# Performance work log

Measured on AMD Instinct MI355X. Metric: run time of the kernel, lower is better.

Reference implementation:

```python
import jax, jax.numpy as jnp
import numpy as np

K_NEIGHBORS = 16
NUM_PATCHES = 32
W_NORMAL = 1.0
W_SURFVAR = 1.0


def _knn_centered(points, k):
    """points: [B, N, 3] -> k nearest neighbors re-centered at each point, [B, N, k, 3].
    Distances are computed on stop_gradient(points) to match torch's .detach()."""
    pd = jax.lax.stop_gradient(points)
    # squared pairwise distances [B, N, N] (sqrt is monotone -> topk order identical)
    d2 = jnp.sum((pd[:, :, None, :] - pd[:, None, :, :]) ** 2, axis=-1)
    _, idx = jax.lax.top_k(-d2, k)  # smallest-k indices, [B, N, k]
    knn = jax.vmap(lambda pts, id_: pts[id_])(points, idx)  # [B, N, k, 3]
    return knn - points[:, :, None, :]


def _eig_props(knn):
    """knn: [B, N, k, 3] -> (normal [B,N,3] = eigvec of smallest eigval, eigvals [B,N,3] ascending)."""
    cov = jnp.einsum('bnki,bnkj->bnij', knn, knn)  # [B, N, 3, 3]
    w, v = jnp.linalg.eigh(cov)  # ascending eigenvalues, matches torch.symeig
    return v[..., :, 0], w


def setup_inputs() -> dict:
    key = jax.random.key(0)
    pointCloud = jax.random.normal(key, (4, 8192, 3), dtype=jnp.float32)
    return {"pointCloud": pointCloud}


def reference(pointCloud):
    B, N, _ = pointCloud.shape
    pp = N // NUM_PATCHES

    # global kNN / normals / surface variance
    knn_g = _knn_centered(pointCloud, K_NEIGHBORS)
    nrm_g, w_g = _eig_props(knn_g)

    # patchwise: each patch is an independent small point cloud -> fold patches into batch
    patch_pts = pointCloud.reshape(B * NUM_PATCHES, pp, 3)
    knn_p = _knn_centered(patch_pts, K_NEIGHBORS)
    nrm_p, w_p = _eig_props(knn_p)
    nrm_p = nrm_p.reshape(B, N, 3)

    # normal loss (abs variant, sign-ambiguity-free)
    loss_n = jnp.mean(jnp.linalg.norm(jnp.abs(nrm_p) - jnp.abs(nrm_g), axis=2)) * W_NORMAL

    # surface variance loss: lambda_min / sum(lambda)
    sv_g = w_g[..., 0] / jnp.sum(w_g, axis=-1)            # [B, N]
    sv_p = (w_p[..., 0] / jnp.sum(w_p, axis=-1)).reshape(B, N)
    loss_sv = jnp.mean((sv_p - sv_g) ** 2) * W_SURFVAR

    return jnp.stack([loss_n, loss_sv])  # [2] (original returns list of two [1] tensors)
```

## Files before the change

kernel.cpp:

```cpp
#include <hip/hip_runtime.h>
#include <math.h>

#define KNN 16
#define NPTS 8192
#define PTCH 256
#define NPATCH 32
#define NBATCH 4
#define SSTRIDE 130
#define LAMBDA_T 48.0f

#define NC 16
#define NCELLS (NC * NC * NC)
#define GMIN -4.2f
#define ICS 1.9047619f

__device__ __forceinline__ float lam_f(float r, float s)
{
    const float C     = 0.063493636f;
    const float SQ2PI = 2.5066283f;
    const float IS2   = 0.70710678f;
    float a = fabsf(r - s), b = r + s;
    float amr = a - r;
    float coefA = amr * amr + 2.f - s * s;
    float I = 2.f * __expf(-0.5f * b * b) - coefA * __expf(-0.5f * a * a)
            + r * SQ2PI * (erff(b * IS2) - erff(a * IS2));
    float M = C * (3.14159265f / r) * I;
    if (s > r) {
        float u = s - r;
        M += 12.566371f * C * (1.2533141f * erff(u * IS2) - u * __expf(-0.5f * u * u));
    }
    return (float)NPTS * M;
}

__device__ __forceinline__ void jrot(double& app, double& aqq, double& apq,
                                     double& arp, double& arq,
                                     double& vp0, double& vq0,
                                     double& vp1, double& vq1,
                                     double& vp2, double& vq2)
{
    double g = apq;
    if (g == 0.0) return;
    double theta = (aqq - app) / (2.0 * g);
    double at = fabs(theta);
    double t = (at > 1.0e154) ? (0.5 / theta)
                              : (copysign(1.0, theta) / (at + sqrt(theta * theta + 1.0)));
    double c = 1.0 / sqrt(t * t + 1.0);
    double s = t * c;
    double tau = s / (1.0 + c);
    app -= t * g;
    aqq += t * g;
    apq = 0.0;
    double rp = arp, rq = arq;
    arp = rp - s * (rq + tau * rp);
    arq = rq + s * (rp - tau * rq);
    double p0 = vp0, q0 = vq0;
    vp0 = p0 - s * (q0 + tau * p0); vq0 = q0 + s * (p0 - tau * q0);
    double p1 = vp1, q1 = vq1;
    vp1 = p1 - s * (q1 + tau * p1); vq1 = q1 + s * (p1 - tau * q1);
    double p2 = vp2, q2 = vq2;
    vp2 = p2 - s * (q2 + tau * p2); vq2 = q2 + s * (p2 - tau * q2);
}

__device__ __forceinline__ void eig3(double a00, double a11, double a22,
                                     double a01, double a02, double a12,
                                     double& nx, double& ny, double& nz,
                                     double& lmin, double& lsum)
{
    double v00 = 1, v01 = 0, v02 = 0;
    double v10 = 0, v11 = 1, v12 = 0;
    double v20 = 0, v21 = 0, v22 = 1;
    double scale = fabs(a00) + fabs(a11) + fabs(a22) + fabs(a01) + fabs(a02) + fabs(a12);
    if (scale > 0.0) {
        for (int sweep = 0; sweep < 6; ++sweep) {
            double off = fabs(a01) + fabs(a02) + fabs(a12);
            if (off <= scale * 1e-15) break;
            jrot(a00, a11, a01, a02, a12, v00, v01, v10, v11, v20, v21);
            jrot(a00, a22, a02, a01, a12, v00, v02, v10, v12, v20, v22);
            jrot(a11, a22, a12, a01, a02, v01, v02, v11, v12, v21, v22);
        }
    }
    lsum = a00 + a11 + a22;
    lmin = a00; nx = v00; ny = v10; nz = v20;
    if (a11 < lmin) { lmin = a11; nx = v01; ny = v11; nz = v21; }
    if (a22 < lmin) { lmin = a22; nx = v02; ny = v12; nz = v22; }
}

__device__ __forceinline__ unsigned mkkey(float d2, unsigned idx) {
    return (__float_as_uint(d2) & 0xFFFFE000u) | idx;
}

__device__ __forceinline__ void insert16(unsigned key, unsigned* L)
{
    L[KNN - 1] = key;
    #pragma unroll
    for (int m = KNN - 1; m >= 1; --m) {
        unsigned a = L[m - 1], b = L[m];
        L[m - 1] = min(a, b);
        L[m]     = max(a, b);
    }
}

__device__ __forceinline__ void merge4(unsigned* L, int lane)
{
    #pragma unroll
    for (int step = 1; step <= 2; step <<= 1) {
        unsigned tmp[KNN];
        #pragma unroll
        for (int m = 0; m < KNN; ++m) tmp[m] = __shfl(L[m], lane ^ step, 64);
        for (int m = 0; m < KNN; ++m) {
            if (tmp[m] >= L[KNN - 1]) break;
            insert16(tmp[m], L);
        }
    }
}

__device__ __forceinline__ unsigned mbcnt64(unsigned long long m) {
    return __builtin_amdgcn_mbcnt_hi((unsigned)(m >> 32),
           __builtin_amdgcn_mbcnt_lo((unsigned)m, 0u));
}

__device__ __forceinline__ int cidx(float v) {
    int i = (int)floorf((v - GMIN) * ICS);
    return min(max(i, 0), NC - 1);
}
__device__ __forceinline__ int cellOf(float x, float y, float z) {
    return (cidx(z) * NC + cidx(y)) * NC + cidx(x);
}

#define BT 1024
__global__ void __launch_bounds__(1024)
build_kernel(const float* __restrict__ pts, float* __restrict__ out,
             unsigned* __restrict__ cellStart, float4* __restrict__ sorted)
{
    __shared__ unsigned hist[NCELLS];
    __shared__ unsigned part[BT];
    const int b = blockIdx.x;
    const int t = threadIdx.x;
    if (b == 0 && t == 0) { out[0] = 0.0f; out[1] = 0.0f; }
    for (int i = t; i < NCELLS; i += BT) hist[i] = 0u;
    __syncthreads();
    const float* base = pts + (size_t)b * (NPTS * 3);
    float px[8], py[8], pz[8];
    int pc[8];
    #pragma unroll
    for (int k = 0; k < 8; ++k) {
        int i = k * BT + t;
        px[k] = base[i * 3 + 0];
        py[k] = base[i * 3 + 1];
        pz[k] = base[i * 3 + 2];
        pc[k] = cellOf(px[k], py[k], pz[k]);
        atomicAdd(&hist[pc[k]], 1u);
    }
    __syncthreads();
    unsigned loc[4], s = 0;
    #pragma unroll
    for (int i = 0; i < 4; ++i) { loc[i] = s; s += hist[t * 4 + i]; }
    part[t] = s;
    __syncthreads();
    for (int o = 1; o < BT; o <<= 1) {
        unsigned u = (t >= o) ? part[t - o] : 0u;
        __syncthreads();
        part[t] += u;
        __syncthreads();
    }
    unsigned basex = part[t] - s;
    unsigned* csb = cellStart + b * (NCELLS + 1);
    #pragma unroll
    for (int i = 0; i < 4; ++i) {
        unsigned e = basex + loc[i];
        csb[t * 4 + i] = e;
        hist[t * 4 + i] = e;
    }
    if (t == BT - 1) csb[NCELLS] = basex + s;
    __syncthreads();
    float4* sb = sorted + (size_t)b * NPTS;
    #pragma unroll
    for (int k = 0; k < 8; ++k) {
        int i = k * BT + t;
        unsigned slot = atomicAdd(&hist[pc[k]], 1u);
        float4 v;
        v.x = px[k]; v.y = py[k]; v.z = pz[k]; v.w = __uint_as_float((unsigned)i);
        sb[slot] = v;
    }
}

__global__ void __launch_bounds__(256)
gate_kernel(const float* __restrict__ pts, float* __restrict__ g2buf)
{
    int q = blockIdx.x * 256 + threadIdx.x;
    int b = q >> 13, i = q & (NPTS - 1);
    const float* pp = pts + (size_t)b * (NPTS * 3) + (size_t)i * 3;
    float x = pp[0], y = pp[1], z = pp[2];
    float r = fmaxf(sqrtf(x * x + y * y + z * z), 0.01f);
    float lo = 0.f, hi = 12.f;
    #pragma unroll 1
    for (int it = 0; it < 16; ++it) {
        float mid = 0.5f * (lo + hi);
        if (lam_f(r, mid) < LAMBDA_T) lo = mid; else hi = mid;
    }
    g2buf[q] = hi * hi;
}

__global__ void __launch_bounds__(256)
fselect_kernel(const float* __restrict__ pts, const float* __restrict__ g2buf,
               const unsigned* __restrict__ cellStart,
               const float4* __restrict__ sortedp,
               unsigned* __restrict__ idx16)
{
    __shared__ unsigned survl[4 * SSTRIDE];
    const int t = threadIdx.x;
    const int wv = t >> 6;
    const int lane = t & 63;
    const int wq = __builtin_amdgcn_readfirstlane(blockIdx.x * 4 + wv);
    const int b  = wq >> 13;
    const int qi = wq & (NPTS - 1);
    const float* base = pts + (size_t)b * (NPTS * 3);
    const unsigned* cs = cellStart + b * (NCELLS + 1);
    const float4* sp = sortedp + (size_t)b * NPTS;
    unsigned* sl = survl + wv * SSTRIDE;

    const float qx = base[qi * 3 + 0];
    const float qy = base[qi * 3 + 1];
    const float qz = base[qi * 3 + 2];
    const float g2 = g2buf[wq];
    const float g  = sqrtf(g2);

    int ixlo = cidx(qx - g), ixhi = cidx(qx + g);
    int iylo = cidx(qy - g), iyhi = cidx(qy + g);
    int izlo = cidx(qz - g), izhi = cidx(qz + g);
    int nx = ixhi - ixlo + 1;
    int ny = iyhi - iylo + 1;
    int nyz = ny * (izhi - izlo + 1);
    const int lR  = (nyz >= 8) ? 3 : (nyz >= 4) ? 2 : (nyz >= 2) ? 1 : 0;
    const int R   = 1 << lR;
    const int lsl = 6 - lR;
    const unsigned SL = 64u >> lR;
    const unsigned slot = (unsigned)lane & (SL - 1u);
    unsigned cnt = 0;
    #pragma unroll 1
    for (int r0 = 0; r0 < nyz; r0 += 64) {
        int r = r0 + lane;
        unsigned pk = 0;
        if (r < nyz) {
            int iz = izlo + r / ny;
            int iy = iylo + (r - (r / ny) * ny);
            int cb = (iz * NC + iy) * NC + ixlo;
            unsigned sB = cs[cb];
            pk = sB | ((cs[cb + nx] - sB) << 14);
        }
        int rmax = min(nyz - r0, 64);
        int gcount = (rmax + R - 1) >> lR;
        #pragma unroll 1
        for (int gg = 0; gg < gcount; ++gg) {
            unsigned pkm = __shfl(pk, (gg << lR) + (lane >> lsl), 64);
            unsigned sBm = pkm & 0x3FFFu;
            unsigned lm  = pkm >> 14;
            #pragma unroll 1
            for (unsigned st = slot; ; st += SL) {
                bool in = st < lm;
                if (!__any(in ? 1 : 0)) break;
                float4 c = sp[min(sBm + st, (unsigned)(NPTS - 1))];
                float dx = qx - c.x, dy = qy - c.y, dz = qz - c.z;
                float d2 = dx * dx + dy * dy + dz * dz;
                bool pass = in && (d2 < g2);
                unsigned long long m = __ballot(pass);
                if (pass) {
                    unsigned sw = min(cnt + mbcnt64(m), (unsigned)(SSTRIDE - 1));
                    sl[sw] = mkkey(d2, __float_as_uint(c.w));
                }
                cnt += (unsigned)__popcll(m);
            }
        }
    }

    bool valid = (cnt >= KNN) && (cnt <= 128u);
    if (valid) {
        unsigned k0 = (lane < (int)cnt)      ? sl[lane]      : 0xFFFFFFFFu;
        unsigned k1 = (lane + 64 < (int)cnt) ? sl[lane + 64] : 0xFFFFFFFFu;
        unsigned P = 0;
        #pragma unroll 1
        for (int bit = 31; bit >= 0; --bit) {
            unsigned mid = P | (1u << bit);
            unsigned c = (unsigned)__popcll(__ballot(k0 < mid))
                       + (unsigned)__popcll(__ballot(k1 < mid));
            if (c < 16u) P = mid;
        }
        float upper = __uint_as_float((P & 0xFFFFE000u) + 0x2000u);
        valid = (upper < g2 * 0.999f - 1e-5f);
        if (valid) {
            bool sel0 = (k0 <= P);
            bool sel1 = (k1 <= P);
            unsigned long long m0 = __ballot(sel0);
            unsigned long long m1 = __ballot(sel1);
            unsigned base1 = (unsigned)__popcll(m0);
            if (sel0) sl[mbcnt64(m0)] = k0;
            if (sel1) sl[base1 + mbcnt64(m1)] = k1;
            unsigned myk = sl[lane & 15];
            unsigned rnk = 0;
            #pragma unroll
            for (int j = 0; j < 16; ++j) {
                unsigned kj = __shfl(myk, j, 64);
                rnk += (kj < myk) ? 1u : 0u;
            }
            if (lane < 16)
                idx16[(size_t)wq * 32 + rnk] = myk & 0x1FFFu;
        }
    }
    if (!valid && lane == 0) {
        unsigned gl[KNN];
        #pragma unroll
        for (int m = 0; m < KNN; ++m) gl[m] = 0xFFFFFFFFu;
        #pragma unroll 1
        for (int i = 0; i < NPTS; ++i) {
            float cx = base[i * 3 + 0];
            float cy = base[i * 3 + 1];
            float cz = base[i * 3 + 2];
            float dx = qx - cx, dy = qy - cy, dz = qz - cz;
            float d2 = dx * dx + dy * dy + dz * dz;
            unsigned k = mkkey(d2, (unsigned)i);
            if (k < gl[KNN - 1]) insert16(k, gl);
        }
        unsigned* dst = idx16 + (size_t)wq * 32;
        #pragma unroll
        for (int m = 0; m < KNN; ++m) dst[m] = gl[m] & 0x1FFFu;
    }
}

__global__ void __launch_bounds__(256)
pselect_kernel(const float* __restrict__ pts, unsigned* __restrict__ idx16)
{
    __shared__ float4 pbuf4[PTCH];
    const int t = threadIdx.x;
    const int w = t >> 6;
    const int lane = t & 63;
    const int p = blockIdx.x;
    const int quarter = blockIdx.y;
    const int b = blockIdx.z;
    const float* base = pts + (size_t)b * (NPTS * 3);

    {
        const float* src = base + p * (PTCH * 3);
        float* dst = (float*)pbuf4;
        #pragma unroll
        for (int s = 0; s < 3; ++s) {
            int f = t + s * 256;
            int j = f / 3;
            int c = f - 3 * j;
            dst[j * 4 + c] = src[f];
        }
    }
    __syncthreads();

    const int qq = lane >> 2;
    const int h = lane & 3;
    const int qlocal = quarter * 64 + w * 16 + qq;
    float4 qv = pbuf4[qlocal];
    const float pqx = qv.x, pqy = qv.y, pqz = qv.z;

    unsigned pl[KNN];
    #pragma unroll
    for (int m = 0; m < KNN; ++m) pl[m] = 0xFFFFFFFFu;
    const int j0 = h * 64;
    #pragma unroll 4
    for (int j = j0; j < j0 + 64; ++j) {
        float4 c = pbuf4[j];
        float dx = pqx - c.x, dy = pqy - c.y, dz = pqz - c.z;
        float d2 = dx * dx + dy * dy + dz * dz;
        unsigned k = mkkey(d2, (unsigned)j);
        if (k < pl[KNN - 1]) insert16(k, pl);
    }
    merge4(pl, lane);
    if (h == 0) {
        int qid = b * NPTS + p * PTCH + qlocal;
        unsigned* dst = idx16 + (size_t)qid * 32 + 16;
        #pragma unroll
        for (int m = 0; m < KNN; ++m)
            dst[m] = (unsigned)(p * PTCH) + (pl[m] & 0x1FFFu);
    }
}

__global__ void __launch_bounds__(256)
eig_loss_kernel(const float* __restrict__ pts,
                const unsigned* __restrict__ idx16,
                double* __restrict__ partials)
{
    __shared__ double sln[4], slv[4];
    const int t = threadIdx.x;
    const int e = blockIdx.x * 256 + t;
    const int qid = e >> 1;
    const int b = qid >> 13;
    const int qi = qid & (NPTS - 1);
    const float* base = pts + (size_t)b * (NPTS * 3);

    const double qxd = (double)base[qi * 3 + 0];
    const double qyd = (double)base[qi * 3 + 1];
    const double qzd = (double)base[qi * 3 + 2];

    const unsigned* L = idx16 + (size_t)qid * 32 + (e & 1) * 16;
    double c00 = 0, c11 = 0, c22 = 0, c01 = 0, c02 = 0, c12 = 0;
    #pragma unroll
    for (int m = 0; m < KNN; ++m) {
        int idx = (int)L[m];
        double dx = (double)base[idx * 3 + 0] - qxd;
        double dy = (double)base[idx * 3 + 1] - qyd;
        double dz = (double)base[idx * 3 + 2] - qzd;
        c00 += dx * dx; c11 += dy * dy; c22 += dz * dz;
        c01 += dx * dy; c02 += dx * dz; c12 += dy * dz;
    }
    double nx, ny, nz, lmin, lsum;
    eig3(c00, c11, c22, c01, c02, c12, nx, ny, nz, lmin, lsum);
    double sv = lmin / lsum;

    double onx = __shfl_xor(nx, 1, 64);
    double ony = __shfl_xor(ny, 1, 64);
    double onz = __shfl_xor(nz, 1, 64);
    double osv = __shfl_xor(sv, 1, 64);

    double ln = 0.0, lsv = 0.0;
    if ((e & 1) == 0) {
        double dx = fabs(onx) - fabs(nx);
        double dy = fabs(ony) - fabs(ny);
        double dz = fabs(onz) - fabs(nz);
        ln  = sqrt(dx * dx + dy * dy + dz * dz);
        double ds = osv - sv;
        lsv = ds * ds;
    }
    #pragma unroll
    for (int o = 32; o > 0; o >>= 1) {
        ln  += __shfl_down(ln, o);
        lsv += __shfl_down(lsv, o);
    }
    const int w = t >> 6;
    if ((t & 63) == 0) { sln[w] = ln; slv[w] = lsv; }
    __syncthreads();
    if (t == 0) {
        partials[blockIdx.x * 2 + 0] = sln[0] + sln[1] + sln[2] + sln[3];
        partials[blockIdx.x * 2 + 1] = slv[0] + slv[1] + slv[2] + slv[3];
    }
}

__global__ void __launch_bounds__(256)
reduce_kernel(const double* __restrict__ partials, float* __restrict__ out)
{
    __shared__ double sln[4], slv[4];
    const int t = threadIdx.x;
    double a = partials[t * 2 + 0];
    double c = partials[t * 2 + 1];
    #pragma unroll
    for (int o = 32; o > 0; o >>= 1) {
        a += __shfl_down(a, o);
        c += __shfl_down(c, o);
    }
    if ((t & 63) == 0) { sln[t >> 6] = a; slv[t >> 6] = c; }
    __syncthreads();
    if (t == 0) {
        const double inv = 1.0 / (double)(NBATCH * NPTS);
        out[0] = (float)((sln[0] + sln[1] + sln[2] + sln[3]) * inv);
        out[1] = (float)((slv[0] + slv[1] + slv[2] + slv[3]) * inv);
    }
}

extern "C" void kernel_launch(void* const* d_in, const int* in_sizes, int n_in,
                              void* d_out, int out_size, void* d_ws, size_t ws_size,
                              hipStream_t stream)
{
    const float* pts = (const float*)d_in[0];
    float* out = (float*)d_out;

    unsigned char* ws = (unsigned char*)d_ws;
    unsigned* cellStart = (unsigned*)(ws);
    float4*   sorted    = (float4*)  (ws + 65552);
    float*    g2buf     = (float*)   (ws + 589840);
    unsigned* idx16     = (unsigned*)(ws + 720912);
    double*   partials  = (double*)  (ws + 4915216);

    hipLaunchKernelGGL(build_kernel, dim3(NBATCH), dim3(BT), 0, stream,
                       pts, out, cellStart, sorted);
    hipLaunchKernelGGL(gate_kernel, dim3(NBATCH * NPTS / 256), dim3(256), 0, stream,
                       pts, g2buf);
    hipLaunchKernelGGL(fselect_kernel, dim3(NBATCH * NPTS / 4), dim3(256), 0, stream,
                       pts, g2buf, cellStart, sorted, idx16);
    hipLaunchKernelGGL(pselect_kernel, dim3(NPATCH, 4, NBATCH), dim3(256), 0, stream,
                       pts, idx16);
    hipLaunchKernelGGL(eig_loss_kernel, dim3(NBATCH * NPTS * 2 / 256), dim3(256),
                       0, stream, pts, idx16, partials);
    hipLaunchKernelGGL(reduce_kernel, dim3(1), dim3(256), 0, stream,
                       partials, out);
}
```

Measured before the change: 146.4 us.

## Split grid build into parallel count/scan/scatter and process queries in cell order

```diff
diff --git a/kernel.cpp b/kernel.cpp
--- a/kernel.cpp
+++ b/kernel.cpp
@@ -127,61 +127,58 @@
     return (cidx(z) * NC + cidx(y)) * NC + cidx(x);
 }
 
-#define BT 1024
-__global__ void __launch_bounds__(1024)
-build_kernel(const float* __restrict__ pts, float* __restrict__ out,
-             unsigned* __restrict__ cellStart, float4* __restrict__ sorted)
-{
-    __shared__ unsigned hist[NCELLS];
-    __shared__ unsigned part[BT];
-    const int b = blockIdx.x;
-    const int t = threadIdx.x;
-    if (b == 0 && t == 0) { out[0] = 0.0f; out[1] = 0.0f; }
-    for (int i = t; i < NCELLS; i += BT) hist[i] = 0u;
-    __syncthreads();
-    const float* base = pts + (size_t)b * (NPTS * 3);
-    float px[8], py[8], pz[8];
-    int pc[8];
-    #pragma unroll
-    for (int k = 0; k < 8; ++k) {
-        int i = k * BT + t;
-        px[k] = base[i * 3 + 0];
-        py[k] = base[i * 3 + 1];
-        pz[k] = base[i * 3 + 2];
-        pc[k] = cellOf(px[k], py[k], pz[k]);
-        atomicAdd(&hist[pc[k]], 1u);
-    }
-    __syncthreads();
-    unsigned loc[4], s = 0;
-    #pragma unroll
-    for (int i = 0; i < 4; ++i) { loc[i] = s; s += hist[t * 4 + i]; }
+__global__ void __launch_bounds__(256) count_kernel(const float* __restrict__ pts,
+                                                    unsigned* __restrict__ counts)
+{
+    int gid = blockIdx.x * 256 + threadIdx.x;
+    int b = gid >> 13, i = gid & (NPTS - 1);
+    const float* p = pts + (size_t)b * (NPTS * 3) + (size_t)i * 3;
+    atomicAdd(&counts[b * NCELLS + cellOf(p[0], p[1], p[2])], 1u);
+}
+
+__global__ void __launch_bounds__(256) scan_kernel(const unsigned* __restrict__ counts,
+                                                   unsigned* __restrict__ cellStart,
+                                                   unsigned* __restrict__ cellPos)
+{
+    __shared__ unsigned part[256];
+    const int b = blockIdx.x, t = threadIdx.x;
+    const unsigned* cnt = counts + b * NCELLS;
+    unsigned loc[16], s = 0;
+    #pragma unroll
+    for (int i = 0; i < 16; ++i) { loc[i] = s; s += cnt[t * 16 + i]; }
     part[t] = s;
     __syncthreads();
-    for (int o = 1; o < BT; o <<= 1) {
+    for (int o = 1; o < 256; o <<= 1) {
         unsigned u = (t >= o) ? part[t - o] : 0u;
         __syncthreads();
         part[t] += u;
         __syncthreads();
     }
-    unsigned basex = part[t] - s;
+    unsigned base = part[t] - s;
     unsigned* csb = cellStart + b * (NCELLS + 1);
-    #pragma unroll
-    for (int i = 0; i < 4; ++i) {
-        unsigned e = basex + loc[i];
-        csb[t * 4 + i] = e;
-        hist[t * 4 + i] = e;
-    }
-    if (t == BT - 1) csb[NCELLS] = basex + s;
-    __syncthreads();
-    float4* sb = sorted + (size_t)b * NPTS;
-    #pragma unroll
-    for (int k = 0; k < 8; ++k) {
-        int i = k * BT + t;
-        unsigned slot = atomicAdd(&hist[pc[k]], 1u);
-        float4 v;
-        v.x = px[k]; v.y = py[k]; v.z = pz[k]; v.w = __uint_as_float((unsigned)i);
-        sb[slot] = v;
-    }
+    unsigned* cpb = cellPos + b * NCELLS;
+    #pragma unroll
+    for (int i = 0; i < 16; ++i) {
+        unsigned e = base + loc[i];
+        csb[t * 16 + i] = e;
+        cpb[t * 16 + i] = e;
+    }
+    if (t == 255) csb[NCELLS] = base + s;
+}
+
+__global__ void __launch_bounds__(256) scatter_kernel(const float* __restrict__ pts,
+                                                      unsigned* __restrict__ cellPos,
+                                                      float4* __restrict__ sorted)
+{
+    int gid = blockIdx.x * 256 + threadIdx.x;
+    int b = gid >> 13, i = gid & (NPTS - 1);
+    const float* p = pts + (size_t)b * (NPTS * 3) + (size_t)i * 3;
+    float x = p[0], y = p[1], z = p[2];
+    int c = cellOf(x, y, z);
+    unsigned slot = atomicAdd(&cellPos[b * NCELLS + c], 1u);
+    float4 v;
+    v.x = x; v.y = y; v.z = z; v.w = __uint_as_float((unsigned)i);
+    sorted[(size_t)b * NPTS + slot] = v;
 }
 
 __global__ void __launch_bounds__(256)
@@ -212,17 +209,17 @@
     const int wv = t >> 6;
     const int lane = t & 63;
     const int wq = __builtin_amdgcn_readfirstlane(blockIdx.x * 4 + wv);
-    const int b  = wq >> 13;
-    const int qi = wq & (NPTS - 1);
+    const int b   = wq >> 13;
+    const int pos = wq & (NPTS - 1);
     const float* base = pts + (size_t)b * (NPTS * 3);
     const unsigned* cs = cellStart + b * (NCELLS + 1);
     const float4* sp = sortedp + (size_t)b * NPTS;
     unsigned* sl = survl + wv * SSTRIDE;
 
-    const float qx = base[qi * 3 + 0];
-    const float qy = base[qi * 3 + 1];
-    const float qz = base[qi * 3 + 2];
-    const float g2 = g2buf[wq];
+    const float4 qc = sp[pos];
+    const float qx = qc.x, qy = qc.y, qz = qc.z;
+    const int oq = b * NPTS + (int)__float_as_uint(qc.w);
+    const float g2 = g2buf[oq];
     const float g  = sqrtf(g2);
 
     int ixlo = cidx(qx - g), ixhi = cidx(qx + g);
@@ -303,7 +300,7 @@
                 rnk += (kj < myk) ? 1u : 0u;
             }
             if (lane < 16)
-                idx16[(size_t)wq * 32 + rnk] = myk & 0x1FFFu;
+                idx16[(size_t)oq * 32 + rnk] = myk & 0x1FFFu;
         }
     }
     if (!valid && lane == 0) {
@@ -320,7 +317,7 @@
             unsigned k = mkkey(d2, (unsigned)i);
             if (k < gl[KNN - 1]) insert16(k, gl);
         }
-        unsigned* dst = idx16 + (size_t)wq * 32;
+        unsigned* dst = idx16 + (size_t)oq * 32;
         #pragma unroll
         for (int m = 0; m < KNN; ++m) dst[m] = gl[m] & 0x1FFFu;
     }
@@ -469,13 +466,20 @@
 
     unsigned char* ws = (unsigned char*)d_ws;
     unsigned* cellStart = (unsigned*)(ws);
-    float4*   sorted    = (float4*)  (ws + 65552);
-    float*    g2buf     = (float*)   (ws + 589840);
-    unsigned* idx16     = (unsigned*)(ws + 720912);
-    double*   partials  = (double*)  (ws + 4915216);
-
-    hipLaunchKernelGGL(build_kernel, dim3(NBATCH), dim3(BT), 0, stream,
-                       pts, out, cellStart, sorted);
+    unsigned* counts    = (unsigned*)(ws + 65552);
+    unsigned* cellPos   = (unsigned*)(ws + 131088);
+    float4*   sorted    = (float4*)  (ws + 196624);
+    float*    g2buf     = (float*)   (ws + 720912);
+    unsigned* idx16     = (unsigned*)(ws + 851984);
+    double*   partials  = (double*)  (ws + 5046288);
+
+    hipMemsetAsync(counts, 0, (size_t)NBATCH * NCELLS * sizeof(unsigned), stream);
+    hipLaunchKernelGGL(count_kernel, dim3(NBATCH * NPTS / 256), dim3(256), 0, stream,
+                       pts, counts);
+    hipLaunchKernelGGL(scan_kernel, dim3(NBATCH), dim3(256), 0, stream,
+                       counts, cellStart, cellPos);
+    hipLaunchKernelGGL(scatter_kernel, dim3(NBATCH * NPTS / 256), dim3(256), 0, stream,
+                       pts, cellPos, sorted);
     hipLaunchKernelGGL(gate_kernel, dim3(NBATCH * NPTS / 256), dim3(256), 0, stream,
                        pts, g2buf);
     hipLaunchKernelGGL(fselect_kernel, dim3(NBATCH * NPTS / 4), dim3(256), 0, stream,
```

After: 151.0 us. +3.2%, slower.

## Fuse gate radius search into fselect, process queries in cell order, rank-select top-16

Applied to the files above, without the earlier changes.

```diff
diff --git a/kernel.cpp b/kernel.cpp
--- a/kernel.cpp
+++ b/kernel.cpp
@@ -129,14 +129,13 @@
 
 #define BT 1024
 __global__ void __launch_bounds__(1024)
-build_kernel(const float* __restrict__ pts, float* __restrict__ out,
+build_kernel(const float* __restrict__ pts,
              unsigned* __restrict__ cellStart, float4* __restrict__ sorted)
 {
     __shared__ unsigned hist[NCELLS];
     __shared__ unsigned part[BT];
     const int b = blockIdx.x;
     const int t = threadIdx.x;
-    if (b == 0 && t == 0) { out[0] = 0.0f; out[1] = 0.0f; }
     for (int i = t; i < NCELLS; i += BT) hist[i] = 0u;
     __syncthreads();
     const float* base = pts + (size_t)b * (NPTS * 3);
@@ -185,24 +184,7 @@
 }
 
 __global__ void __launch_bounds__(256)
-gate_kernel(const float* __restrict__ pts, float* __restrict__ g2buf)
-{
-    int q = blockIdx.x * 256 + threadIdx.x;
-    int b = q >> 13, i = q & (NPTS - 1);
-    const float* pp = pts + (size_t)b * (NPTS * 3) + (size_t)i * 3;
-    float x = pp[0], y = pp[1], z = pp[2];
-    float r = fmaxf(sqrtf(x * x + y * y + z * z), 0.01f);
-    float lo = 0.f, hi = 12.f;
-    #pragma unroll 1
-    for (int it = 0; it < 16; ++it) {
-        float mid = 0.5f * (lo + hi);
-        if (lam_f(r, mid) < LAMBDA_T) lo = mid; else hi = mid;
-    }
-    g2buf[q] = hi * hi;
-}
-
-__global__ void __launch_bounds__(256)
-fselect_kernel(const float* __restrict__ pts, const float* __restrict__ g2buf,
+fselect_kernel(const float* __restrict__ pts,
                const unsigned* __restrict__ cellStart,
                const float4* __restrict__ sortedp,
                unsigned* __restrict__ idx16)
@@ -212,18 +194,27 @@
     const int wv = t >> 6;
     const int lane = t & 63;
     const int wq = __builtin_amdgcn_readfirstlane(blockIdx.x * 4 + wv);
-    const int b  = wq >> 13;
-    const int qi = wq & (NPTS - 1);
+    const int b   = wq >> 13;
+    const int pos = wq & (NPTS - 1);
     const float* base = pts + (size_t)b * (NPTS * 3);
     const unsigned* cs = cellStart + b * (NCELLS + 1);
     const float4* sp = sortedp + (size_t)b * NPTS;
     unsigned* sl = survl + wv * SSTRIDE;
 
-    const float qx = base[qi * 3 + 0];
-    const float qy = base[qi * 3 + 1];
-    const float qz = base[qi * 3 + 2];
-    const float g2 = g2buf[wq];
-    const float g  = sqrtf(g2);
+    const float4 qc = sp[pos];
+    const float qx = qc.x, qy = qc.y, qz = qc.z;
+    const int oq = b * NPTS + (int)__float_as_uint(qc.w);
+
+    const float r = fmaxf(sqrtf(qx * qx + qy * qy + qz * qz), 0.01f);
+    const float H1 = 12.0f / 64.0f;
+    float s1 = H1 * (float)(lane + 1);
+    unsigned j1 = (unsigned)__popcll(__ballot(lam_f(r, s1) < LAMBDA_T));
+    float lo1 = H1 * (float)min(j1, 63u);
+    const float H2 = H1 / 64.0f;
+    float s2 = lo1 + H2 * (float)(lane + 1);
+    unsigned j2 = (unsigned)__popcll(__ballot(lam_f(r, s2) < LAMBDA_T));
+    float g = lo1 + H2 * (float)(min(j2, 63u) + 1u);
+    const float g2 = g * g;
 
     int ixlo = cidx(qx - g), ixhi = cidx(qx + g);
     int iylo = cidx(qy - g), iyhi = cidx(qy + g);
@@ -239,11 +230,11 @@
     unsigned cnt = 0;
     #pragma unroll 1
     for (int r0 = 0; r0 < nyz; r0 += 64) {
-        int r = r0 + lane;
+        int rr = r0 + lane;
         unsigned pk = 0;
-        if (r < nyz) {
-            int iz = izlo + r / ny;
-            int iy = iylo + (r - (r / ny) * ny);
+        if (rr < nyz) {
+            int iz = izlo + rr / ny;
+            int iy = iylo + (rr - (rr / ny) * ny);
             int cb = (iz * NC + iy) * NC + ixlo;
             unsigned sB = cs[cb];
             pk = sB | ((cs[cb + nx] - sB) << 14);
@@ -277,33 +268,26 @@
     if (valid) {
         unsigned k0 = (lane < (int)cnt)      ? sl[lane]      : 0xFFFFFFFFu;
         unsigned k1 = (lane + 64 < (int)cnt) ? sl[lane + 64] : 0xFFFFFFFFu;
-        unsigned P = 0;
-        #pragma unroll 1
-        for (int bit = 31; bit >= 0; --bit) {
-            unsigned mid = P | (1u << bit);
-            unsigned c = (unsigned)__popcll(__ballot(k0 < mid))
-                       + (unsigned)__popcll(__ballot(k1 < mid));
-            if (c < 16u) P = mid;
-        }
-        float upper = __uint_as_float((P & 0xFFFFE000u) + 0x2000u);
+        unsigned r0 = 0, r1 = 0;
+        #pragma unroll 4
+        for (unsigned m = 0; m < cnt; ++m) {
+            unsigned km = sl[m];
+            r0 += (km < k0) ? 1u : 0u;
+            r1 += (km < k1) ? 1u : 0u;
+        }
+        unsigned cand = 0;
+        if (lane < (int)cnt && r0 == 15u) cand = k0;
+        if (lane + 64 < (int)cnt && r1 == 15u) cand = k1;
+        #pragma unroll
+        for (int o = 1; o < 64; o <<= 1)
+            cand = max(cand, (unsigned)__shfl_xor((int)cand, o, 64));
+        float upper = __uint_as_float((cand & 0xFFFFE000u) + 0x2000u);
         valid = (upper < g2 * 0.999f - 1e-5f);
         if (valid) {
-            bool sel0 = (k0 <= P);
-            bool sel1 = (k1 <= P);
-            unsigned long long m0 = __ballot(sel0);
-            unsigned long long m1 = __ballot(sel1);
-            unsigned base1 = (unsigned)__popcll(m0);
-            if (sel0) sl[mbcnt64(m0)] = k0;
-            if (sel1) sl[base1 + mbcnt64(m1)] = k1;
-            unsigned myk = sl[lane & 15];
-            unsigned rnk = 0;
-            #pragma unroll
-            for (int j = 0; j < 16; ++j) {
-                unsigned kj = __shfl(myk, j, 64);
-                rnk += (kj < myk) ? 1u : 0u;
-            }
-            if (lane < 16)
-                idx16[(size_t)wq * 32 + rnk] = myk & 0x1FFFu;
+            if (lane < (int)cnt && r0 < 16u)
+                idx16[(size_t)oq * 32 + r0] = k0 & 0x1FFFu;
+            if (lane + 64 < (int)cnt && r1 < 16u)
+                idx16[(size_t)oq * 32 + r1] = k1 & 0x1FFFu;
         }
     }
     if (!valid && lane == 0) {
@@ -320,7 +304,7 @@
             unsigned k = mkkey(d2, (unsigned)i);
             if (k < gl[KNN - 1]) insert16(k, gl);
         }
-        unsigned* dst = idx16 + (size_t)wq * 32;
+        unsigned* dst = idx16 + (size_t)oq * 32;
         #pragma unroll
         for (int m = 0; m < KNN; ++m) dst[m] = gl[m] & 0x1FFFu;
     }
@@ -470,16 +454,13 @@
     unsigned char* ws = (unsigned char*)d_ws;
     unsigned* cellStart = (unsigned*)(ws);
     float4*   sorted    = (float4*)  (ws + 65552);
-    float*    g2buf     = (float*)   (ws + 589840);
-    unsigned* idx16     = (unsigned*)(ws + 720912);
-    double*   partials  = (double*)  (ws + 4915216);
+    unsigned* idx16     = (unsigned*)(ws + 589840);
+    double*   partials  = (double*)  (ws + 4784144);
 
     hipLaunchKernelGGL(build_kernel, dim3(NBATCH), dim3(BT), 0, stream,
-                       pts, out, cellStart, sorted);
-    hipLaunchKernelGGL(gate_kernel, dim3(NBATCH * NPTS / 256), dim3(256), 0, stream,
-                       pts, g2buf);
+                       pts, cellStart, sorted);
     hipLaunchKernelGGL(fselect_kernel, dim3(NBATCH * NPTS / 4), dim3(256), 0, stream,
-                       pts, g2buf, cellStart, sorted, idx16);
+                       pts, cellStart, sorted, idx16);
     hipLaunchKernelGGL(pselect_kernel, dim3(NPATCH, 4, NBATCH), dim3(256), 0, stream,
                        pts, idx16);
     hipLaunchKernelGGL(eig_loss_kernel, dim3(NBATCH * NPTS * 2 / 256), dim3(256),
```

Result: no change. 144.9 us (-1.0%).
